# Performance work log

Hardware: AMD Instinct MI355X
Metric: run time of the kernel (lower is better)

## Reference

```python
import jax, jax.numpy as jnp
import numpy as np

H = 768
NHEADS = 2
MAX_REL = 96  # module's max_rel_enc; static here (positive count >> 96 for these inputs)


def _ln(x, g, b, eps=1e-5):
    m = jnp.mean(x, axis=-1, keepdims=True)
    v = jnp.var(x, axis=-1, keepdims=True)
    return (x - m) * jax.lax.rsqrt(v + eps) * g + b


def _mha(q, k, v, in_w, in_b, out_w, out_b, key_pad):
    # q [B,Lq,H], k/v [B,Lk,H], key_pad [B,Lk] bool (True = masked key)
    d = q.shape[-1]
    dh = d // NHEADS
    wq, wk, wv = jnp.split(in_w, 3, axis=0)
    bq, bk, bv = jnp.split(in_b, 3)
    qh = (q @ wq.T + bq).reshape(q.shape[0], q.shape[1], NHEADS, dh)
    kh = (k @ wk.T + bk).reshape(k.shape[0], k.shape[1], NHEADS, dh)
    vh = (v @ wv.T + bv).reshape(v.shape[0], v.shape[1], NHEADS, dh)
    scores = jnp.einsum('bqhd,bkhd->bhqk', qh, kh) / np.float32(np.sqrt(dh))
    scores = jnp.where(key_pad[:, None, None, :], jnp.float32(-1e9), scores)
    attn = jax.nn.softmax(scores, axis=-1)
    out = jnp.einsum('bhqk,bkhd->bqhd', attn, vh).reshape(q.shape)
    return out @ out_w.T + out_b


def _forward(hidden_states, logits_prev, block_mask, W_rel, b_rel,
             enc_in_w, enc_in_b, enc_out_w, enc_out_b,
             enc_l1_w, enc_l1_b, enc_l2_w, enc_l2_b,
             enc_ln1_g, enc_ln1_b, enc_ln2_g, enc_ln2_b,
             dec_in_w, dec_in_b, dec_out_w, dec_out_b,
             dec_l1_w, dec_l1_b, dec_l2_w, dec_l2_b,
             dec_ln1_g, dec_ln1_b, dec_ln2_g, dec_ln2_b,
             fc_w, fc_b):
    B, N, Hd = hidden_states.shape
    # rel_layer(cat([h_i, h_j])) == h_i @ Wa.T + h_j @ Wb.T + b  (avoids [B,N,N,2H] intermediate)
    Wa = W_rel[:, :Hd]
    Wb = W_rel[:, Hd:]
    A = hidden_states @ Wa.T   # [B,N,H]
    C = hidden_states @ Wb.T   # [B,N,H]
    feat_pair = (A[:, :, None, :] + C[:, None, :, :] + b_rel).reshape(B, N * N, Hd)

    bm = block_mask.astype(jnp.float32)
    pair_mask = (bm[:, :, None] * bm[:, None, :]).reshape(B, N * N)
    score = jax.nn.sigmoid(logits_prev).reshape(B, N * N)
    neg = (score < 0.5).astype(jnp.float32)
    neg = 1.0 - (1.0 - neg) * pair_mask           # 1 = negative-or-invalid pair
    neg = jax.lax.stop_gradient(neg)              # matches score_prev.detach_()

    # dynamic top-k gather of positive pairs (static MAX_REL here)
    idx = jnp.argsort(neg, axis=1)[:, :MAX_REL]                     # positives (neg==0) first
    enc_pad = jnp.take_along_axis(neg, idx, axis=1) > 0.5           # [B,MAX_REL]
    enc_pad = enc_pad.at[:, 0].set(False)
    feat_now = feat_pair * (1.0 - neg)[:, :, None]
    pos_pairs = jnp.take_along_axis(feat_now, idx[:, :, None], axis=1)  # [B,MAX_REL,H]

    # 1-layer transformer encoder (post-norm, ReLU, d_ff = H)
    x = pos_pairs
    x = _ln(x + _mha(x, x, x, enc_in_w, enc_in_b, enc_out_w, enc_out_b, enc_pad),
            enc_ln1_g, enc_ln1_b)
    ff = jax.nn.relu(x @ enc_l1_w.T + enc_l1_b) @ enc_l2_w.T + enc_l2_b
    patterns = _ln(x + ff, enc_ln2_g, enc_ln2_b)

    # 1-layer decoder with self_attn=False: cross-attn + FFN, post-norm
    t = feat_pair
    t = _ln(t + _mha(t, patterns, patterns, dec_in_w, dec_in_b, dec_out_w, dec_out_b, enc_pad),
            dec_ln1_g, dec_ln1_b)
    ff = jax.nn.relu(t @ dec_l1_w.T + dec_l1_b) @ dec_l2_w.T + dec_l2_b
    t = _ln(t + ff, dec_ln2_g, dec_ln2_b)

    refined = t.reshape(B, N, N, Hd)
    return (refined @ fc_w.T + fc_b)[..., 0]    # [B,N,N]


def setup_inputs() -> dict:
    key = jax.random.key(0)
    ks = jax.random.split(key, 24)
    B, N = 4, 128
    p = lambda k, s: jax.random.normal(k, s, jnp.float32) * 0.02
    return {
        'hidden_states': jax.random.normal(ks[0], (B, N, H), jnp.float32),
        'logits_prev': jax.random.normal(ks[1], (B, N, N), jnp.float32),
        'block_mask': jax.random.randint(ks[2], (B, N), 0, 2),
        'W_rel': p(ks[3], (H, 2 * H)), 'b_rel': p(ks[4], (H,)),
        'enc_in_w': p(ks[5], (3 * H, H)), 'enc_in_b': p(ks[6], (3 * H,)),
        'enc_out_w': p(ks[7], (H, H)), 'enc_out_b': p(ks[8], (H,)),
        'enc_l1_w': p(ks[9], (H, H)), 'enc_l1_b': p(ks[10], (H,)),
        'enc_l2_w': p(ks[11], (H, H)), 'enc_l2_b': p(ks[12], (H,)),
        'enc_ln1_g': jnp.ones((H,), jnp.float32), 'enc_ln1_b': jnp.zeros((H,), jnp.float32),
        'enc_ln2_g': jnp.ones((H,), jnp.float32), 'enc_ln2_b': jnp.zeros((H,), jnp.float32),
        'dec_in_w': p(ks[13], (3 * H, H)), 'dec_in_b': p(ks[14], (3 * H,)),
        'dec_out_w': p(ks[15], (H, H)), 'dec_out_b': p(ks[16], (H,)),
        'dec_l1_w': p(ks[17], (H, H)), 'dec_l1_b': p(ks[18], (H,)),
        'dec_l2_w': p(ks[19], (H, H)), 'dec_l2_b': p(ks[20], (H,)),
        'dec_ln1_g': jnp.ones((H,), jnp.float32), 'dec_ln1_b': jnp.zeros((H,), jnp.float32),
        'dec_ln2_g': jnp.ones((H,), jnp.float32), 'dec_ln2_b': jnp.zeros((H,), jnp.float32),
        'fc_w': p(ks[21], (1, H)), 'fc_b': p(ks[22], (1,)),
    }


def reference(hidden_states, logits_prev, block_mask, W_rel, b_rel,
              enc_in_w, enc_in_b, enc_out_w, enc_out_b,
              enc_l1_w, enc_l1_b, enc_l2_w, enc_l2_b,
              enc_ln1_g, enc_ln1_b, enc_ln2_g, enc_ln2_b,
              dec_in_w, dec_in_b, dec_out_w, dec_out_b,
              dec_l1_w, dec_l1_b, dec_l2_w, dec_l2_b,
              dec_ln1_g, dec_ln1_b, dec_ln2_g, dec_ln2_b,
              fc_w, fc_b):
    return _forward(hidden_states, logits_prev, block_mask, W_rel, b_rel,
                    enc_in_w, enc_in_b, enc_out_w, enc_out_b,
                    enc_l1_w, enc_l1_b, enc_l2_w, enc_l2_b,
                    enc_ln1_g, enc_ln1_b, enc_ln2_g, enc_ln2_b,
                    dec_in_w, dec_in_b, dec_out_w, dec_out_b,
                    dec_l1_w, dec_l1_b, dec_l2_w, dec_l2_b,
                    dec_ln1_g, dec_ln1_b, dec_ln2_g, dec_ln2_b,
                    fc_w, fc_b)
```

## Files before the change

### kernel.cpp

```cpp
#include <hip/hip_runtime.h>
#include <cstdint>
#include <cstddef>

typedef unsigned short u16;
typedef __attribute__((ext_vector_type(8))) short sv8;
typedef __attribute__((ext_vector_type(4))) short sv4;
typedef __attribute__((ext_vector_type(4))) float fv4;
typedef __attribute__((ext_vector_type(8))) __bf16 bv8;

#define WAITVM(N) asm volatile("s_waitcnt vmcnt(" #N ")" ::: "memory")
#define WAITLG0() asm volatile("s_waitcnt lgkmcnt(0)" ::: "memory")
#define SB0() __builtin_amdgcn_sched_barrier(0)
#define BAR() __builtin_amdgcn_s_barrier()

__device__ __forceinline__ float b2f(u16 u) {
  union { unsigned int i; float f; } v; v.i = ((unsigned int)u) << 16; return v.f;
}
__device__ __forceinline__ u16 f2b(float f) {
  union { float f; unsigned int i; } v; v.f = f;
  unsigned int r = v.i + 0x7fffu + ((v.i >> 16) & 1u);
  return (u16)(r >> 16);
}

__device__ __forceinline__ void gload16(const u16* g, u16* l) {
  __builtin_amdgcn_global_load_lds(
      (const __attribute__((address_space(1))) void*)g,
      (__attribute__((address_space(3))) void*)l, 16, 0, 0);
}

struct CvtArgs { const float* src[10]; u16* dst[10]; int n[10]; };

__global__ __launch_bounds__(256) void cvt_multi(CvtArgs a) {
  int t = blockIdx.y;
  const float* s = a.src[t];
  u16* d = a.dst[t];
  int n = a.n[t];
  int i4 = (blockIdx.x * 256 + threadIdx.x) * 4;
  if (i4 + 4 <= n) {
    float4 v = *(const float4*)(s + i4);
    sv4 o;
    o[0] = (short)f2b(v.x); o[1] = (short)f2b(v.y);
    o[2] = (short)f2b(v.z); o[3] = (short)f2b(v.w);
    *(sv4*)(d + i4) = o;
  }
}

__global__ __launch_bounds__(256) void prep_q0(
    const float* __restrict__ dec_in_w, const float* __restrict__ dec_in_b,
    const float* __restrict__ b_rel, float* __restrict__ q0) {
  int wave = threadIdx.x >> 6, lane = threadIdx.x & 63;
  int row = blockIdx.x * 4 + wave;
  const float* wrp = dec_in_w + (size_t)row * 768;
  float acc = 0.f;
  #pragma unroll
  for (int t = 0; t < 3; t++) {
    float4 wv = *(const float4*)(wrp + (t * 64 + lane) * 4);
    float4 bv = *(const float4*)(b_rel + (t * 64 + lane) * 4);
    acc += wv.x * bv.x + wv.y * bv.y + wv.z * bv.z + wv.w * bv.w;
  }
  #pragma unroll
  for (int d = 1; d <= 32; d <<= 1) acc += __shfl_xor(acc, d);
  if (lane == 0) q0[row] = acc + dec_in_b[row];
}

__global__ __launch_bounds__(256) void prep_q0k(
    const float* __restrict__ q0, const u16* __restrict__ khb,
    float* __restrict__ q0k) {
  int wave = threadIdx.x >> 6, lane = threadIdx.x & 63;
  int idx = blockIdx.x * 4 + wave;
  int b = idx / 192, c = idx % 192;
  int h = (c < 96) ? 0 : 1;
  int k = (c < 96) ? c : c - 96;
  const u16* kr = khb + ((size_t)(b * 96 + k)) * 768 + h * 384;
  const float* qp = q0 + h * 384;
  float acc = 0.f;
  #pragma unroll
  for (int t = 0; t < 6; t++) {
    int d = t * 64 + lane;
    acc += qp[d] * b2f(kr[d]);
  }
  #pragma unroll
  for (int d = 1; d <= 32; d <<= 1) acc += __shfl_xor(acc, d);
  if (lane == 0) q0k[idx] = acc * 0.05103103630798287f;
}

__global__ __launch_bounds__(256) void prep_misc(
    const float* __restrict__ dec_out_b, const float* __restrict__ b_rel,
    const float* __restrict__ ln2g, const float* __restrict__ ln2b,
    const float* __restrict__ fc_w, const float* __restrict__ fc_b,
    float* __restrict__ bb, float* __restrict__ gfc, float* __restrict__ scal) {
  int tid = threadIdx.x;
  int wave = tid >> 6, lane = tid & 63;
  float s1 = 0.f, s2 = 0.f;
  for (int t = tid; t < 768; t += 256) {
    bb[t] = dec_out_b[t] + b_rel[t];
    float gf = ln2g[t] * fc_w[t];
    gfc[t] = gf;
    s1 += gf; s2 += ln2b[t] * fc_w[t];
  }
  #pragma unroll
  for (int d = 1; d <= 32; d <<= 1) { s1 += __shfl_xor(s1, d); s2 += __shfl_xor(s2, d); }
  __shared__ float r1[4], r2[4];
  if (lane == 0) { r1[wave] = s1; r2[wave] = s2; }
  __syncthreads();
  if (tid == 0) {
    float a = r1[0] + r1[1] + r1[2] + r1[3];
    float c = r2[0] + r2[1] + r2[2] + r2[3];
    scal[1] = a;
    scal[0] = c + fc_b[0];
  }
}

__global__ __launch_bounds__(256) void select_pairs(
    const float* __restrict__ logits, const int* __restrict__ bm,
    int* __restrict__ idxb, int* __restrict__ encpad, int* __restrict__ zflag) {
  int b = blockIdx.x, tid = threadIdx.x;
  int wave = tid >> 6, lane = tid & 63;
  __shared__ unsigned char pos[16384];
  __shared__ int bml[128];
  __shared__ int wsum[4];
  const float* lg = logits + (size_t)b * 16384;
  if (tid < 128) bml[tid] = bm[b * 128 + tid];
  __syncthreads();
  for (int i = 0; i < 16; i++) {
    int e4 = (i * 256 + tid) * 4;
    float4 v = *(const float4*)(lg + e4);
    uchar4 o;
    {
      float sg = 1.f / (1.f + expf(-v.x));
      o.x = (!(sg < 0.5f)) && bml[e4 >> 7] && bml[e4 & 127];
      sg = 1.f / (1.f + expf(-v.y));
      o.y = (!(sg < 0.5f)) && bml[(e4 + 1) >> 7] && bml[(e4 + 1) & 127];
      sg = 1.f / (1.f + expf(-v.z));
      o.z = (!(sg < 0.5f)) && bml[(e4 + 2) >> 7] && bml[(e4 + 2) & 127];
      sg = 1.f / (1.f + expf(-v.w));
      o.w = (!(sg < 0.5f)) && bml[(e4 + 3) >> 7] && bml[(e4 + 3) & 127];
    }
    *(uchar4*)(pos + e4) = o;
  }
  __syncthreads();
  int cnt = 0;
  #pragma unroll 8
  for (int u = 0; u < 64; u++) cnt += pos[tid * 64 + u];
  int v = cnt;
  #pragma unroll
  for (int d = 1; d < 64; d <<= 1) { int o = __shfl_up(v, d); if (lane >= d) v += o; }
  if (lane == 63) wsum[wave] = v;
  __syncthreads();
  int wbase = 0;
  for (int w = 0; w < wave; w++) wbase += wsum[w];
  int mtot = wsum[0] + wsum[1] + wsum[2] + wsum[3];
  int pq = wbase + v - cnt;
  int nq = tid * 64 - pq;
  for (int u = 0; u < 64; u++) {
    int p = tid * 64 + u;
    if (pos[p]) {
      if (pq < 96) { idxb[b * 96 + pq] = p; encpad[b * 96 + pq] = 0; zflag[b * 96 + pq] = 0; }
      pq++;
    } else {
      int slot = mtot + nq;
      if (slot < 96) { idxb[b * 96 + slot] = p; encpad[b * 96 + slot] = 1; zflag[b * 96 + slot] = 1; }
      nq++;
    }
  }
  __syncthreads();
  if (tid == 0) encpad[b * 96] = 0;
}

__global__ __launch_bounds__(256) void gather_pp(
    const float* __restrict__ Af, const float* __restrict__ Cf,
    const float* __restrict__ b_rel, const int* __restrict__ idxb,
    const int* __restrict__ zflag, u16* __restrict__ PP) {
  int s = blockIdx.x, b = blockIdx.y;
  int slot = b * 96 + s;
  int p = idxb[slot];
  int z = zflag[slot];
  const float* ar = Af + ((size_t)b * 128 + (p >> 7)) * 768;
  const float* cr = Cf + ((size_t)b * 128 + (p & 127)) * 768;
  for (int c = threadIdx.x; c < 768; c += 256) {
    float v = z ? 0.f : (ar[c] + cr[c] + b_rel[c]);
    PP[(size_t)slot * 768 + c] = f2b(v);
  }
}

template<int EPI, int OUTM, int BM>
__global__ __launch_bounds__(256) void gemm_bt(
    const u16* __restrict__ Aptr, const u16* __restrict__ Wptr,
    const float* __restrict__ bias,
    void* __restrict__ out1, void* __restrict__ out2,
    const u16* __restrict__ resp, int ldr,
    int M, int N, int K, int lda, int ldw, int ldo,
    int ZH, int zbm, int bstr,
    long sAb, long sAh, long sWb, long sWh, long sOb, long sOh,
    float scale) {
  constexpr int FR = BM / 32;
  constexpr int BUF = BM * 32;
  int z = blockIdx.z;
  int zb = z / ZH, zh = z % ZH;
  const u16* A = Aptr + (size_t)zb * sAb + (size_t)zh * sAh;
  const u16* W = Wptr + (size_t)(zb & zbm) * sWb + (size_t)zh * sWh;
  const float* bz = bias ? bias + (size_t)zb * bstr : nullptr;
  size_t obase = (size_t)zb * sOb + (size_t)zh * sOh;

  int m0 = blockIdx.x * BM, n0 = blockIdx.y * BM;
  int tid = threadIdx.x;
  int wave = tid >> 6, lane = tid & 63;
  int wr = (wave >> 1) * (BM / 2), wc = (wave & 1) * (BM / 2);

  __shared__ __attribute__((aligned(16))) u16 As[4 * BUF];
  __shared__ __attribute__((aligned(16))) u16 Ws[4 * BUF];

  fv4 acc[FR][FR] = {};

  int srow = tid & (BM - 1);
  int scol = (BM == 128) ? ((tid >> 7) * 8) : ((tid >> 6) * 8);
  int ra = m0 + srow; if (ra > M - 1) ra = M - 1;
  int rw = n0 + srow; if (rw > N - 1) rw = N - 1;
  const u16* gA = A + (size_t)ra * lda + scol;
  const u16* gW = W + (size_t)rw * ldw + scol;
  int lofs = wave * 512;

  int rb = (lane >> 4) * (BM * 8) + (lane & 15) * 8;

  int nt = K >> 5;

  auto stage = [&](int tile) {
    int k0 = tile << 5;
    int cu = tile & 3;
    u16* la = As + cu * BUF + lofs;
    u16* lw = Ws + cu * BUF + lofs;
    gload16(gA + k0, la);
    gload16(gW + k0, lw);
    if (BM == 128) {
      gload16(gA + k0 + 16, la + 2048);
      gload16(gW + k0 + 16, lw + 2048);
    }
  };

  auto compute = [&](int cu) {
    const u16* Ap = As + cu * BUF;
    const u16* Wp = Ws + cu * BUF;
    bv8 af[FR], wf[FR];
    #pragma unroll
    for (int f = 0; f < FR; f++) af[f] = *(const bv8*)(Ap + rb + (wr + f * 16) * 8);
    #pragma unroll
    for (int f = 0; f < FR; f++) wf[f] = *(const bv8*)(Wp + rb + (wc + f * 16) * 8);
    __builtin_amdgcn_s_setprio(1);
    #pragma unroll
    for (int fm = 0; fm < FR; fm++)
      #pragma unroll
      for (int fn = 0; fn < FR; fn++)
        acc[fm][fn] = __builtin_amdgcn_mfma_f32_16x16x32_bf16(af[fm], wf[fn], acc[fm][fn], 0, 0, 0);
    __builtin_amdgcn_s_setprio(0);
  };

  stage(0); stage(1); stage(2);

  for (int t = 0; t < nt - 3; ++t) {
    if constexpr (BM == 128) WAITVM(8); else WAITVM(4);
    BAR();
    stage(t + 3);
    SB0();
    compute(t & 3);
  }
  { if constexpr (BM == 128) WAITVM(8); else WAITVM(4); BAR(); SB0(); compute((nt - 3) & 3); }
  { if constexpr (BM == 128) WAITVM(4); else WAITVM(2); BAR(); SB0(); compute((nt - 2) & 3); }
  { WAITVM(0); BAR(); SB0(); compute((nt - 1) & 3); }

  int lr4 = (lane >> 4) * 4, lc = lane & 15;
  #pragma unroll
  for (int fm = 0; fm < FR; fm++) {
    #pragma unroll
    for (int r = 0; r < 4; r++) {
      int row = m0 + wr + fm * 16 + lr4 + r;
      if (row >= M) continue;
      #pragma unroll
      for (int fn = 0; fn < FR; fn++) {
        int col = n0 + wc + fn * 16 + lc;
        if (col >= N) continue;
        float v = acc[fm][fn][r] * scale;
        if (bz) v += bz[col];
        if (EPI == 1) v = fmaxf(v, 0.f);
        if (EPI == 2) v += b2f(resp[(size_t)row * ldr + col]);
        size_t o = obase + (size_t)row * ldo + col;
        if (OUTM == 0) ((u16*)out1)[o] = f2b(v);
        else if (OUTM == 1) ((float*)out1)[o] = v;
        else { ((float*)out1)[o] = v; ((u16*)out2)[o] = f2b(v); }
      }
    }
  }
}

template<int EPI>
__global__ __launch_bounds__(512, 2) void gemm256(
    const u16* __restrict__ Aptr, const u16* __restrict__ Wptr,
    const float* __restrict__ bias, u16* __restrict__ out,
    const u16* __restrict__ resp, int ldr,
    const float* __restrict__ exA, const float* __restrict__ exC,
    int K, int lda, int ldw, int ldo,
    long zA, long zW, long zO, long zR, long zE) {
  __shared__ __attribute__((aligned(16))) u16 lds[4 * 2 * 8192];

  int nwg = gridDim.x * gridDim.y * gridDim.z;
  int lin = blockIdx.x + gridDim.x * (blockIdx.y + gridDim.y * blockIdx.z);
  int q8 = nwg >> 3;
  int swz = (lin & 7) * q8 + (lin >> 3);
  int bx = swz & 63;
  int rest = swz >> 6;
  int by = rest % 3;
  int zz = rest / 3;

  const u16* A = Aptr + (size_t)zz * zA;
  const u16* W = Wptr + (size_t)zz * zW;
  u16* outz = out + (size_t)zz * zO;
  const u16* respz = resp + (size_t)zz * zR;
  const float* exAz = exA + (size_t)zz * zE;
  const float* exCz = exC + (size_t)zz * zE;

  int m0 = bx * 256, n0 = by * 256;
  int tid = threadIdx.x;
  int wave = tid >> 6, lane = tid & 63;
  int wr = (wave >> 2) * 128;
  int wc = (wave & 3) * 64;
  int lr = lane & 15, ls = lane >> 4;

  const u16* gAbase = A + (size_t)(m0 + (tid & 255)) * lda + (tid >> 8) * 8;
  const u16* gWbase = W + (size_t)(n0 + (tid & 255)) * ldw + (tid >> 8) * 8;
  int ldest0 = wave * 512;

  fv4 acc[8][4] = {};

  auto stageu = [&](int h3, int T, int c) {
    u16* dest = lds + ((h3 & 3) * 16384 + T * 8192 + c * 4096 + ldest0);
    const u16* g = (T == 0 ? gAbase : gWbase) + h3 * 32 + c * 16;
    gload16(g, dest);
  };

  int TH = K >> 5;
  #pragma unroll
  for (int h3 = 0; h3 < 3; ++h3) {
    stageu(h3, 0, 0); stageu(h3, 0, 1); stageu(h3, 1, 0); stageu(h3, 1, 1);
  }
  WAITVM(8);
  BAR();

  for (int h = 0; h < TH; ++h) {
    const u16* Ah = lds + (h & 3) * 16384;
    const u16* Wh = Ah + 8192;
    int hs = h + 3;
    bool st = hs < TH;
    bv8 wf[4], af[4];
    #pragma unroll
    for (int n = 0; n < 4; n++) wf[n] = *(const bv8*)(Wh + ls * 2048 + (wc + n * 16 + lr) * 8);
    #pragma unroll
    for (int f = 0; f < 4; f++) af[f] = *(const bv8*)(Ah + ls * 2048 + (wr + f * 16 + lr) * 8);
    if (st) { stageu(hs, 0, 0); stageu(hs, 0, 1); }
    BAR();
    WAITLG0(); SB0();
    __builtin_amdgcn_s_setprio(1);
    #pragma unroll
    for (int f = 0; f < 4; f++)
      #pragma unroll
      for (int n = 0; n < 4; n++)
        acc[f][n] = __builtin_amdgcn_mfma_f32_16x16x32_bf16(af[f], wf[n], acc[f][n], 0, 0, 0);
    __builtin_amdgcn_s_setprio(0);
    BAR();
    #pragma unroll
    for (int f = 0; f < 4; f++) af[f] = *(const bv8*)(Ah + ls * 2048 + (wr + 64 + f * 16 + lr) * 8);
    if (st) { stageu(hs, 1, 0); stageu(hs, 1, 1); }
    BAR();
    WAITLG0(); SB0();
    __builtin_amdgcn_s_setprio(1);
    #pragma unroll
    for (int f = 0; f < 4; f++)
      #pragma unroll
      for (int n = 0; n < 4; n++)
        acc[4 + f][n] = __builtin_amdgcn_mfma_f32_16x16x32_bf16(af[f], wf[n], acc[4 + f][n], 0, 0, 0);
    __builtin_amdgcn_s_setprio(0);
    int rem = TH - 2 - h;
    if (rem >= 2) { WAITVM(8); }
    else if (rem == 1) { WAITVM(4); }
    else { WAITVM(0); }
    BAR();
  }

  int lr4 = (lane >> 4) * 4, lc = lane & 15;
  #pragma unroll
  for (int fm = 0; fm < 8; fm++) {
    #pragma unroll
    for (int r = 0; r < 4; r++) {
      int row = m0 + wr + (fm >> 2) * 64 + (fm & 3) * 16 + lr4 + r;
      #pragma unroll
      for (int fn = 0; fn < 4; fn++) {
        int col = n0 + wc + fn * 16 + lc;
        float v = acc[fm][fn][r] + bias[col];
        if (EPI == 1) v = fmaxf(v, 0.f);
        if (EPI == 2) v += b2f(respz[(size_t)row * ldr + col]);
        if (EPI == 3) v += exAz[(size_t)(row >> 7) * 768 + col] + exCz[(size_t)(row & 127) * 768 + col];
        outz[(size_t)row * ldo + col] = f2b(v);
      }
    }
  }
}

__global__ __launch_bounds__(128) void enc_att(
    const u16* __restrict__ QKV, const int* __restrict__ encpad, u16* __restrict__ AO) {
  int s = blockIdx.x;
  int bh = blockIdx.y;
  int b = bh >> 1, h = bh & 1;
  int tid = threadIdx.x;
  __shared__ float q[384];
  __shared__ float sc[96];
  __shared__ float red[2];
  size_t rowq = ((size_t)b * 96 + s) * 2304;
  for (int d = tid; d < 384; d += 128) q[d] = b2f(QKV[rowq + h * 384 + d]);
  __syncthreads();
  if (tid < 96) {
    const u16* kr = QKV + ((size_t)b * 96 + tid) * 2304 + 768 + h * 384;
    float acc = 0.f;
    for (int d = 0; d < 384; d++) acc += q[d] * b2f(kr[d]);
    acc *= 0.05103103630798287f;
    if (encpad[b * 96 + tid]) acc = -1e9f;
    sc[tid] = acc;
  }
  __syncthreads();
  if (tid == 0) {
    float m = sc[0];
    for (int k = 1; k < 96; k++) m = fmaxf(m, sc[k]);
    red[0] = m;
  }
  __syncthreads();
  if (tid < 96) sc[tid] = __expf(sc[tid] - red[0]);
  __syncthreads();
  if (tid == 0) {
    float sum = 0.f;
    for (int k = 0; k < 96; k++) sum += sc[k];
    red[1] = 1.f / sum;
  }
  __syncthreads();
  float inv = red[1];
  for (int d = tid; d < 384; d += 128) {
    const u16* vb = QKV + (size_t)b * 96 * 2304 + 1536 + h * 384 + d;
    float acc = 0.f;
    for (int k = 0; k < 96; k++) acc += sc[k] * b2f(vb[(size_t)k * 2304]);
    AO[((size_t)b * 96 + s) * 768 + h * 384 + d] = f2b(acc * inv);
  }
}

__global__ __launch_bounds__(256) void softmax_pairs(
    const float* __restrict__ SA, const float* __restrict__ SC,
    const float* __restrict__ q0k,
    const int* __restrict__ encpad, u16* __restrict__ P) {
  int wave = threadIdx.x >> 6, lane = threadIdx.x & 63;
  int bi = blockIdx.y;
  int p = blockIdx.x * 4 + wave;
  int i = p >> 7, j = p & 127;
  const float* sa = SA + ((size_t)bi * 128 + i) * 192;
  const float* sc = SC + ((size_t)bi * 128 + j) * 192;
  const float* qk = q0k + bi * 192;
  int c0 = lane * 3;
  float s0, s1, s2;
  {
    int c = c0;     int k = (c < 96) ? c : c - 96;
    s0 = encpad[bi * 96 + k] ? -1e9f : (sa[c] + sc[c] + qk[c]);
    c = c0 + 1;     k = (c < 96) ? c : c - 96;
    s1 = encpad[bi * 96 + k] ? -1e9f : (sa[c] + sc[c] + qk[c]);
    c = c0 + 2;     k = (c < 96) ? c : c - 96;
    s2 = encpad[bi * 96 + k] ? -1e9f : (sa[c] + sc[c] + qk[c]);
  }
  float m = fmaxf(s0, fmaxf(s1, s2));
  #pragma unroll
  for (int d = 1; d <= 16; d <<= 1) m = fmaxf(m, __shfl_xor(m, d));
  float e0 = __expf(s0 - m), e1 = __expf(s1 - m), e2 = __expf(s2 - m);
  float sum = e0 + e1 + e2;
  #pragma unroll
  for (int d = 1; d <= 16; d <<= 1) sum += __shfl_xor(sum, d);
  float inv = 1.f / sum;
  u16* o = P + ((size_t)bi * 16384 + p) * 192 + c0;
  o[0] = f2b(e0 * inv); o[1] = f2b(e1 * inv); o[2] = f2b(e2 * inv);
}

__global__ __launch_bounds__(256) void ln_rows(
    const u16* __restrict__ Y, const float* __restrict__ g,
    const float* __restrict__ bt, u16* __restrict__ X, int rows) {
  int wave = threadIdx.x >> 6, lane = threadIdx.x & 63;
  int row = blockIdx.x * 4 + wave;
  if (row >= rows) return;
  const u16* y = Y + (size_t)row * 768;
  sv8 v1 = *(const sv8*)(y + lane * 8);
  sv4 v2 = *(const sv4*)(y + 512 + lane * 4);
  float x[12];
  #pragma unroll
  for (int t = 0; t < 8; t++) x[t] = b2f((u16)v1[t]);
  #pragma unroll
  for (int t = 0; t < 4; t++) x[8 + t] = b2f((u16)v2[t]);
  float s = 0.f, q = 0.f;
  #pragma unroll
  for (int t = 0; t < 12; t++) { s += x[t]; q += x[t] * x[t]; }
  #pragma unroll
  for (int d = 1; d <= 32; d <<= 1) { s += __shfl_xor(s, d); q += __shfl_xor(q, d); }
  float mean = s * (1.f / 768.f);
  float var = q * (1.f / 768.f) - mean * mean;
  float rstd = rsqrtf(var + 1e-5f);
  u16* xo = X + (size_t)row * 768;
  sv8 w1; sv4 w2;
  #pragma unroll
  for (int t = 0; t < 8; t++) {
    int c = lane * 8 + t;
    w1[t] = (short)f2b((x[t] - mean) * rstd * g[c] + bt[c]);
  }
  #pragma unroll
  for (int t = 0; t < 4; t++) {
    int c = 512 + lane * 4 + t;
    w2[t] = (short)f2b((x[8 + t] - mean) * rstd * g[c] + bt[c]);
  }
  *(sv8*)(xo + lane * 8) = w1;
  *(sv4*)(xo + 512 + lane * 4) = w2;
}

__global__ __launch_bounds__(256) void final_rows(
    const u16* __restrict__ Y, const float* __restrict__ gfc,
    const float* __restrict__ scal, float* __restrict__ out, int rows) {
  int wave = threadIdx.x >> 6, lane = threadIdx.x & 63;
  int row = blockIdx.x * 4 + wave;
  if (row >= rows) return;
  const u16* y = Y + (size_t)row * 768;
  sv8 v1 = *(const sv8*)(y + lane * 8);
  sv4 v2 = *(const sv4*)(y + 512 + lane * 4);
  float x[12];
  #pragma unroll
  for (int t = 0; t < 8; t++) x[t] = b2f((u16)v1[t]);
  #pragma unroll
  for (int t = 0; t < 4; t++) x[8 + t] = b2f((u16)v2[t]);
  float s = 0.f, q = 0.f, sg = 0.f;
  #pragma unroll
  for (int t = 0; t < 8; t++) {
    int c = lane * 8 + t;
    s += x[t]; q += x[t] * x[t]; sg += x[t] * gfc[c];
  }
  #pragma unroll
  for (int t = 0; t < 4; t++) {
    int c = 512 + lane * 4 + t;
    s += x[8 + t]; q += x[8 + t] * x[8 + t]; sg += x[8 + t] * gfc[c];
  }
  #pragma unroll
  for (int d = 1; d <= 32; d <<= 1) {
    s += __shfl_xor(s, d); q += __shfl_xor(q, d); sg += __shfl_xor(sg, d);
  }
  float mean = s * (1.f / 768.f);
  float var = q * (1.f / 768.f) - mean * mean;
  float rstd = rsqrtf(var + 1e-5f);
  if (lane == 0) out[row] = rstd * (sg - mean * scal[1]) + scal[0];
}

extern "C" void kernel_launch(void* const* d_in, const int* in_sizes, int n_in,
                              void* d_out, int out_size, void* d_ws, size_t ws_size,
                              hipStream_t stream) {
  (void)in_sizes; (void)n_in; (void)out_size;
  const float* hs        = (const float*)d_in[0];
  const float* logits    = (const float*)d_in[1];
  const int*   bmask     = (const int*)d_in[2];
  const float* W_rel     = (const float*)d_in[3];
  const float* b_rel     = (const float*)d_in[4];
  const float* enc_in_w  = (const float*)d_in[5];
  const float* enc_in_b  = (const float*)d_in[6];
  const float* enc_out_w = (const float*)d_in[7];
  const float* enc_out_b = (const float*)d_in[8];
  const float* enc_l1_w  = (const float*)d_in[9];
  const float* enc_l1_b  = (const float*)d_in[10];
  const float* enc_l2_w  = (const float*)d_in[11];
  const float* enc_l2_b  = (const float*)d_in[12];
  const float* enc_ln1_g = (const float*)d_in[13];
  const float* enc_ln1_b = (const float*)d_in[14];
  const float* enc_ln2_g = (const float*)d_in[15];
  const float* enc_ln2_b = (const float*)d_in[16];
  const float* dec_in_w  = (const float*)d_in[17];
  const float* dec_in_b  = (const float*)d_in[18];
  const float* dec_out_w = (const float*)d_in[19];
  const float* dec_out_b = (const float*)d_in[20];
  const float* dec_l1_w  = (const float*)d_in[21];
  const float* dec_l1_b  = (const float*)d_in[22];
  const float* dec_l2_w  = (const float*)d_in[23];
  const float* dec_l2_b  = (const float*)d_in[24];
  const float* dec_ln1_g = (const float*)d_in[25];
  const float* dec_ln1_b = (const float*)d_in[26];
  const float* dec_ln2_g = (const float*)d_in[27];
  const float* dec_ln2_b = (const float*)d_in[28];
  const float* fc_w      = (const float*)d_in[29];
  const float* fc_b      = (const float*)d_in[30];

  char* base = (char*)d_ws;
  size_t off = 0;
  auto alloc = [&](size_t bytes) -> void* {
    size_t o = (off + 255) & ~(size_t)255;
    off = o + bytes;
    return (void*)(base + o);
  };

  u16* hsb   = (u16*)alloc((size_t)393216 * 2);
  u16* wrelb = (u16*)alloc((size_t)1179648 * 2);
  u16* eiwb  = (u16*)alloc((size_t)1769472 * 2);
  u16* eowb  = (u16*)alloc((size_t)589824 * 2);
  u16* el1b  = (u16*)alloc((size_t)589824 * 2);
  u16* el2b  = (u16*)alloc((size_t)589824 * 2);
  u16* diwb  = (u16*)alloc((size_t)1769472 * 2);
  u16* dowb  = (u16*)alloc((size_t)589824 * 2);
  u16* dl1b  = (u16*)alloc((size_t)589824 * 2);
  u16* dl2b  = (u16*)alloc((size_t)589824 * 2);
  float* Af  = (float*)alloc((size_t)786432 * 4);
  float* Cf  = Af + 393216;
  u16* ACb   = (u16*)alloc((size_t)786432 * 2);
  float* q0  = (float*)alloc(768 * 4);
  float* q0k = (float*)alloc(768 * 4);
  float* bbv = (float*)alloc(768 * 4);
  float* gfc = (float*)alloc(768 * 4);
  float* scal = (float*)alloc(4 * 4);
  int* idxb   = (int*)alloc(384 * 4);
  int* encpadb = (int*)alloc(384 * 4);
  int* zflagb  = (int*)alloc(384 * 4);
  u16* PPb   = (u16*)alloc((size_t)294912 * 2);
  u16* QKVe  = (u16*)alloc((size_t)884736 * 2);
  u16* AOe   = (u16*)alloc((size_t)294912 * 2);
  u16* Ye    = (u16*)alloc((size_t)294912 * 2);
  u16* Xe    = (u16*)alloc((size_t)294912 * 2);
  u16* He    = (u16*)alloc((size_t)294912 * 2);
  u16* Y2e   = (u16*)alloc((size_t)294912 * 2);
  u16* patternsb = (u16*)alloc((size_t)294912 * 2);
  u16* khb   = (u16*)alloc((size_t)294912 * 2);
  u16* vhb   = (u16*)alloc((size_t)294912 * 2);
  u16* AqCqb = (u16*)alloc((size_t)786432 * 2);
  float* SASCf = (float*)alloc((size_t)196608 * 4);
  u16* VOTb  = (u16*)alloc((size_t)589824 * 2);
  u16* Pb    = (u16*)alloc((size_t)12582912 * 2);

  const size_t ACT1 = (size_t)12582912 * 2;
  size_t fixed = (off + 255) & ~(size_t)255;
  int NB = 1;
  if (fixed + 2 * 4 * ACT1 + 4096 <= ws_size) NB = 4;
  else if (fixed + 2 * 2 * ACT1 + 4096 <= ws_size) NB = 2;
  u16* Y1buf = (u16*)alloc((size_t)NB * 12582912 * 2);
  u16* H1buf = (u16*)alloc((size_t)NB * 12582912 * 2);

  CvtArgs ca{};
  int ci = 0;
  auto addc = [&](const float* s, u16* d, int n) { ca.src[ci] = s; ca.dst[ci] = d; ca.n[ci] = n; ci++; };
  addc(hs, hsb, 393216);        addc(W_rel, wrelb, 1179648);
  addc(enc_in_w, eiwb, 1769472); addc(enc_out_w, eowb, 589824);
  addc(enc_l1_w, el1b, 589824);  addc(enc_l2_w, el2b, 589824);
  addc(dec_in_w, diwb, 1769472); addc(dec_out_w, dowb, 589824);
  addc(dec_l1_w, dl1b, 589824);  addc(dec_l2_w, dl2b, 589824);
  cvt_multi<<<dim3(1728, 10, 1), 256, 0, stream>>>(ca);

  prep_q0<<<192, 256, 0, stream>>>(dec_in_w, dec_in_b, b_rel, q0);
  prep_misc<<<1, 256, 0, stream>>>(dec_out_b, b_rel, dec_ln2_g, dec_ln2_b, fc_w, fc_b,
                                   bbv, gfc, scal);
  select_pairs<<<dim3(4, 1, 1), 256, 0, stream>>>(logits, bmask, idxb, encpadb, zflagb);

  gemm_bt<0, 2, 64><<<dim3(8, 12, 2), 256, 0, stream>>>(hsb, wrelb, nullptr, Af, ACb,
      nullptr, 0, 512, 768, 768, 768, 1536, 768,
      1, -1, 0, 0, 0, 768, 0, 393216, 0, 1.f);

  gather_pp<<<dim3(96, 4, 1), 256, 0, stream>>>(Af, Cf, b_rel, idxb, zflagb, PPb);

  gemm_bt<0, 0, 64><<<dim3(6, 36, 1), 256, 0, stream>>>(PPb, eiwb, enc_in_b, QKVe, nullptr,
      nullptr, 0, 384, 2304, 768, 768, 768, 2304,
      1, -1, 0, 0, 0, 0, 0, 0, 0, 1.f);
  enc_att<<<dim3(96, 8, 1), 128, 0, stream>>>(QKVe, encpadb, AOe);
  gemm_bt<2, 0, 64><<<dim3(6, 12, 1), 256, 0, stream>>>(AOe, eowb, enc_out_b, Ye, nullptr,
      PPb, 768, 384, 768, 768, 768, 768, 768,
      1, -1, 0, 0, 0, 0, 0, 0, 0, 1.f);
  ln_rows<<<96, 256, 0, stream>>>(Ye, enc_ln1_g, enc_ln1_b, Xe, 384);
  gemm_bt<1, 0, 64><<<dim3(6, 12, 1), 256, 0, stream>>>(Xe, el1b, enc_l1_b, He, nullptr,
      nullptr, 0, 384, 768, 768, 768, 768, 768,
      1, -1, 0, 0, 0, 0, 0, 0, 0, 1.f);
  gemm_bt<2, 0, 64><<<dim3(6, 12, 1), 256, 0, stream>>>(He, el2b, enc_l2_b, Y2e, nullptr,
      Xe, 768, 384, 768, 768, 768, 768, 768,
      1, -1, 0, 0, 0, 0, 0, 0, 0, 1.f);
  ln_rows<<<96, 256, 0, stream>>>(Y2e, enc_ln2_g, enc_ln2_b, patternsb, 384);

  gemm_bt<0, 0, 64><<<dim3(6, 12, 2), 256, 0, stream>>>(patternsb, diwb + (size_t)768 * 768,
      dec_in_b + 768, khb, nullptr, nullptr, 0,
      384, 768, 768, 768, 768, 768,
      1, -1, 768, 0, 0, 589824, 0, 294912, 0, 1.f);
  prep_q0k<<<192, 256, 0, stream>>>(q0, khb, q0k);
  gemm_bt<0, 0, 64><<<dim3(16, 12, 1), 256, 0, stream>>>(ACb, diwb, nullptr, AqCqb, nullptr,
      nullptr, 0, 1024, 768, 768, 768, 768, 768,
      1, -1, 0, 0, 0, 0, 0, 0, 0, 1.f);
  const float scl = 0.05103103630798287f;
  gemm_bt<0, 1, 64><<<dim3(2, 2, 16), 256, 0, stream>>>(AqCqb, khb, nullptr, SASCf, nullptr,
      nullptr, 0, 128, 96, 384, 768, 768, 192,
      2, 3, 0, 98304, 384, 73728, 384, 24576, 96, scl);
  gemm_bt<0, 0, 64><<<dim3(12, 2, 8), 256, 0, stream>>>(dowb, vhb, nullptr, VOTb, nullptr,
      nullptr, 0, 768, 96, 384, 768, 768, 192,
      2, -1, 0, 0, 384, 73728, 384, 147456, 96, 1.f);

  softmax_pairs<<<dim3(4096, 4), 256, 0, stream>>>(SASCf, SASCf + 98304, q0k, encpadb, Pb);
  const long PB_B = 3145728, VOT_B = 147456, ACT_B = 12582912, EX_B = 98304;
  for (int g = 0; g < 4; g += NB) {
    gemm256<3><<<dim3(64, 3, NB), 512, 0, stream>>>(
        Pb + (size_t)g * PB_B, VOTb + (size_t)g * VOT_B, bbv, Y1buf,
        Y1buf, 0, Af + (size_t)g * EX_B, Cf + (size_t)g * EX_B,
        192, 192, 192, 768, PB_B, VOT_B, ACT_B, 0, EX_B);
    ln_rows<<<NB * 4096, 256, 0, stream>>>(Y1buf, dec_ln1_g, dec_ln1_b, Y1buf, NB * 16384);
    gemm256<1><<<dim3(64, 3, NB), 512, 0, stream>>>(
        Y1buf, dl1b, dec_l1_b, H1buf, H1buf, 0, Af, Cf,
        768, 768, 768, 768, ACT_B, 0, ACT_B, 0, 0);
    gemm256<2><<<dim3(64, 3, NB), 512, 0, stream>>>(
        H1buf, dl2b, dec_l2_b, Y1buf, Y1buf, 768, Af, Cf,
        768, 768, 768, 768, ACT_B, 0, ACT_B, ACT_B, 0);
    final_rows<<<NB * 4096, 256, 0, stream>>>(Y1buf, gfc, scal,
        (float*)d_out + (size_t)g * 16384, NB * 16384);
  }
}
```

Before: 624.4 us.

## Restructure gemm256 to double-buffered K=64 tiles with XOR-swizzled LDS layout

```diff
diff --git a/kernel.cpp b/kernel.cpp
--- a/kernel.cpp
+++ b/kernel.cpp
@@ -299,7 +299,7 @@
     const float* __restrict__ exA, const float* __restrict__ exC,
     int K, int lda, int ldw, int ldo,
     long zA, long zW, long zO, long zR, long zE) {
-  __shared__ __attribute__((aligned(16))) u16 lds[4 * 2 * 8192];
+  __shared__ __attribute__((aligned(16))) u16 lds[2 * 2 * 16384];
 
   int nwg = gridDim.x * gridDim.y * gridDim.z;
   int lin = blockIdx.x + gridDim.x * (blockIdx.y + gridDim.y * blockIdx.z);
@@ -323,39 +323,45 @@
   int wr = (wave >> 2) * 128;
   int wc = (wave & 3) * 64;
   int lr = lane & 15, ls = lane >> 4;
-
-  const u16* gAbase = A + (size_t)(m0 + (tid & 255)) * lda + (tid >> 8) * 8;
-  const u16* gWbase = W + (size_t)(n0 + (tid & 255)) * ldw + (tid >> 8) * 8;
-  int ldest0 = wave * 512;
+  int axor = lr & 7;
+
+  int srow = tid >> 3;
+  int schunk = (tid & 7) ^ (srow & 7);
+  const u16* gA0 = A + (size_t)(m0 + srow) * lda + schunk * 8;
+  const u16* gW0 = W + (size_t)(n0 + srow) * ldw + schunk * 8;
+  int wofs = wave * 512;
 
   fv4 acc[8][4] = {};
 
-  auto stageu = [&](int h3, int T, int c) {
-    u16* dest = lds + ((h3 & 3) * 16384 + T * 8192 + c * 4096 + ldest0);
-    const u16* g = (T == 0 ? gAbase : gWbase) + h3 * 32 + c * 16;
-    gload16(g, dest);
+  auto stageA = [&](int t, int q) {
+    gload16(gA0 + (size_t)q * 64 * lda + t * 64,
+            lds + (t & 1) * 32768 + q * 4096 + wofs);
   };
-
-  int TH = K >> 5;
-  #pragma unroll
-  for (int h3 = 0; h3 < 3; ++h3) {
-    stageu(h3, 0, 0); stageu(h3, 0, 1); stageu(h3, 1, 0); stageu(h3, 1, 1);
-  }
-  WAITVM(8);
+  auto stageW = [&](int t, int q) {
+    gload16(gW0 + (size_t)q * 64 * ldw + t * 64,
+            lds + (t & 1) * 32768 + 16384 + q * 4096 + wofs);
+  };
+
+  int TH = K >> 6;
+  #pragma unroll
+  for (int q = 0; q < 4; q++) stageA(0, q);
+  #pragma unroll
+  for (int q = 0; q < 4; q++) stageW(0, q);
+  WAITVM(0);
   BAR();
 
-  for (int h = 0; h < TH; ++h) {
-    const u16* Ah = lds + (h & 3) * 16384;
-    const u16* Wh = Ah + 8192;
-    int hs = h + 3;
-    bool st = hs < TH;
-    bv8 wf[4], af[4];
-    #pragma unroll
-    for (int n = 0; n < 4; n++) wf[n] = *(const bv8*)(Wh + ls * 2048 + (wc + n * 16 + lr) * 8);
-    #pragma unroll
-    for (int f = 0; f < 4; f++) af[f] = *(const bv8*)(Ah + ls * 2048 + (wr + f * 16 + lr) * 8);
-    if (st) { stageu(hs, 0, 0); stageu(hs, 0, 1); }
-    BAR();
+  for (int t = 0; t < TH; ++t) {
+    const u16* Ab = lds + (t & 1) * 32768;
+    const u16* Wb = Ab + 16384;
+    bool st = (t + 1 < TH);
+    bv8 af[4], wf[4];
+    #pragma unroll
+    for (int n = 0; n < 4; n++)
+      wf[n] = *(const bv8*)(Wb + (wc + n * 16 + lr) * 64 + (ls ^ axor) * 8);
+    #pragma unroll
+    for (int f = 0; f < 4; f++)
+      af[f] = *(const bv8*)(Ab + (wr + f * 16 + lr) * 64 + (ls ^ axor) * 8);
+    if (st) { stageA(t + 1, 0); stageA(t + 1, 1); }
     WAITLG0(); SB0();
     __builtin_amdgcn_s_setprio(1);
     #pragma unroll
@@ -364,11 +370,10 @@
       for (int n = 0; n < 4; n++)
         acc[f][n] = __builtin_amdgcn_mfma_f32_16x16x32_bf16(af[f], wf[n], acc[f][n], 0, 0, 0);
     __builtin_amdgcn_s_setprio(0);
-    BAR();
-    #pragma unroll
-    for (int f = 0; f < 4; f++) af[f] = *(const bv8*)(Ah + ls * 2048 + (wr + 64 + f * 16 + lr) * 8);
-    if (st) { stageu(hs, 1, 0); stageu(hs, 1, 1); }
-    BAR();
+    #pragma unroll
+    for (int f = 0; f < 4; f++)
+      af[f] = *(const bv8*)(Ab + (wr + 64 + f * 16 + lr) * 64 + (ls ^ axor) * 8);
+    if (st) { stageA(t + 1, 2); stageA(t + 1, 3); stageW(t + 1, 0); }
     WAITLG0(); SB0();
     __builtin_amdgcn_s_setprio(1);
     #pragma unroll
@@ -377,10 +382,33 @@
       for (int n = 0; n < 4; n++)
         acc[4 + f][n] = __builtin_amdgcn_mfma_f32_16x16x32_bf16(af[f], wf[n], acc[4 + f][n], 0, 0, 0);
     __builtin_amdgcn_s_setprio(0);
-    int rem = TH - 2 - h;
-    if (rem >= 2) { WAITVM(8); }
-    else if (rem == 1) { WAITVM(4); }
-    else { WAITVM(0); }
+    #pragma unroll
+    for (int n = 0; n < 4; n++)
+      wf[n] = *(const bv8*)(Wb + (wc + n * 16 + lr) * 64 + ((ls + 4) ^ axor) * 8);
+    #pragma unroll
+    for (int f = 0; f < 4; f++)
+      af[f] = *(const bv8*)(Ab + (wr + f * 16 + lr) * 64 + ((ls + 4) ^ axor) * 8);
+    if (st) { stageW(t + 1, 1); stageW(t + 1, 2); stageW(t + 1, 3); }
+    WAITLG0(); SB0();
+    __builtin_amdgcn_s_setprio(1);
+    #pragma unroll
+    for (int f = 0; f < 4; f++)
+      #pragma unroll
+      for (int n = 0; n < 4; n++)
+        acc[f][n] = __builtin_amdgcn_mfma_f32_16x16x32_bf16(af[f], wf[n], acc[f][n], 0, 0, 0);
+    __builtin_amdgcn_s_setprio(0);
+    #pragma unroll
+    for (int f = 0; f < 4; f++)
+      af[f] = *(const bv8*)(Ab + (wr + 64 + f * 16 + lr) * 64 + ((ls + 4) ^ axor) * 8);
+    WAITLG0(); SB0();
+    __builtin_amdgcn_s_setprio(1);
+    #pragma unroll
+    for (int f = 0; f < 4; f++)
+      #pragma unroll
+      for (int n = 0; n < 4; n++)
+        acc[4 + f][n] = __builtin_amdgcn_mfma_f32_16x16x32_bf16(af[f], wf[n], acc[4 + f][n], 0, 0, 0);
+    __builtin_amdgcn_s_setprio(0);
+    if (st) WAITVM(0);
     BAR();
   }
 
```

After: 522.5 us. -16.3%, faster.
